# Performance work log

Measured on AMD Instinct MI355X. Metric: run time of the kernel, lower is better.

## Reference

```python
import jax, jax.numpy as jnp
import numpy as np

N_QUBITS = 16
N_LAYERS = 6
BATCH = 512


def _apply_1q(state, U, q, n, batched):
    """Apply a single-qubit gate U to qubit q of state (B, 2**n).
    U: (2,2) shared, or (B,2,2) per-sample if batched."""
    B = state.shape[0]
    d0, d1 = 2 ** q, 2 ** (n - q - 1)
    s = state.reshape(B, d0, 2, d1)
    if batched:
        s = jnp.einsum('bij,bxjy->bxiy', U, s)
    else:
        s = jnp.einsum('ij,bxjy->bxiy', U, s)
    return s.reshape(B, -1)


def _apply_cnot(state, c, t, n):
    """CNOT with control c, target t on state (B, 2**n)."""
    B = state.shape[0]
    a, b = (c, t) if c < t else (t, c)
    d0, d1, d2 = 2 ** a, 2 ** (b - a - 1), 2 ** (n - b - 1)
    s = state.reshape(B, d0, 2, d1, 2, d2)
    if c < t:  # control = axis 2, target = axis 4: flip target where control==1
        s = jnp.concatenate([s[:, :, :1], jnp.flip(s[:, :, 1:], axis=4)], axis=2)
    else:      # control = axis 4, target = axis 2
        s = jnp.concatenate([s[:, :, :, :, :1], jnp.flip(s[:, :, :, :, 1:], axis=2)], axis=4)
    return s.reshape(B, -1)


def _rx(theta):
    """RX(theta) for a batch of angles -> (B,2,2) complex64."""
    c = jnp.cos(theta * 0.5).astype(jnp.complex64)
    s = (-1j * jnp.sin(theta * 0.5)).astype(jnp.complex64)
    return jnp.stack([jnp.stack([c, s], -1), jnp.stack([s, c], -1)], -2)


def _rot(phi, theta, omega):
    """PennyLane Rot(phi,theta,omega) = RZ(omega) RY(theta) RZ(phi) -> (2,2) complex64."""
    c = jnp.cos(theta * 0.5)
    s = jnp.sin(theta * 0.5)
    m00 = jnp.exp(-0.5j * (phi + omega)) * c
    m01 = -jnp.exp(0.5j * (phi - omega)) * s
    m10 = jnp.exp(-0.5j * (phi - omega)) * s
    m11 = jnp.exp(0.5j * (phi + omega)) * c
    return jnp.stack([jnp.stack([m00, m01]), jnp.stack([m10, m11])]).astype(jnp.complex64)


def _circuit(x, weights, n, n_layers):
    B = x.shape[0]
    state = jnp.zeros((B, 2 ** n), dtype=jnp.complex64).at[:, 0].set(1.0)
    # AngleEmbedding: default rotation is RX(x_q) on wire q (per-sample angles)
    for q in range(n):
        state = _apply_1q(state, _rx(x[:, q]), q, n, batched=True)
    # StronglyEntanglingLayers: Rot on each wire, then ring of CNOTs with range r
    for l in range(n_layers):
        for q in range(n):
            U = _rot(weights[l, q, 0], weights[l, q, 1], weights[l, q, 2])
            state = _apply_1q(state, U, q, n, batched=False)
        r = (l % (n - 1)) + 1  # PennyLane default ranges
        for q in range(n):
            state = _apply_cnot(state, q, (q + r) % n, n)
    # <Z_q> = P(bit_q = 0) - P(bit_q = 1)
    probs = state.real ** 2 + state.imag ** 2  # (B, 2**n)
    exps = []
    for q in range(n):
        p = probs.reshape(B, 2 ** q, 2, -1).sum(axis=(1, 3))  # (B, 2)
        exps.append(p[:, 0] - p[:, 1])
    return jnp.stack(exps, axis=-1)  # (B, n)


def setup_inputs() -> dict:
    key = jax.random.key(0)
    kx, kw = jax.random.split(key)
    x = jax.random.normal(kx, (BATCH, N_QUBITS), dtype=jnp.float32)
    weights = jax.random.normal(kw, (N_LAYERS, N_QUBITS, 3), dtype=jnp.float32)
    return {"x": x, "weights": weights}


def reference(x, weights):
    return _circuit(x, weights, N_QUBITS, N_LAYERS)
```

## Files before the change

### kernel.cpp

```cpp
#include <hip/hip_runtime.h>


#define NTH 512
typedef float v32f __attribute__((ext_vector_type(32)));

template <int I> struct IC { static constexpr int value = I; };
template <int N, int I = 0, typename F>
__device__ __forceinline__ void static_for(F&& f) {
  if constexpr (I < N) { f(IC<I>{}); static_for<N, I + 1>(f); }
}


template <int LB>
__device__ __forceinline__ void rot_local(v32f& ar, v32f& ai, const float* __restrict__ u) {
  const float u00r = u[0], u00i = u[1], u01r = u[2], u01i = u[3];
  const float u10r = u[4], u10i = u[5], u11r = u[6], u11i = u[7];
  static_for<16>([&](auto hc) {
    constexpr int h = hc.value;
    constexpr int e0 = ((h >> LB) << (LB + 1)) | (h & ((1 << LB) - 1));
    constexpr int e1 = e0 | (1 << LB);
    const float axr = ar[e0], axi = ai[e0], bxr = ar[e1], bxi = ai[e1];
    ar[e0] = u00r * axr - u00i * axi + u01r * bxr - u01i * bxi;
    ai[e0] = u00r * axi + u00i * axr + u01r * bxi + u01i * bxr;
    ar[e1] = u10r * axr - u10i * axi + u11r * bxr - u11i * bxi;
    ai[e1] = u10r * axi + u10i * axr + u11r * bxi + u11i * bxr;
  });
}

__device__ __forceinline__ void rot_lane(v32f& ar, v32f& ai, const float* __restrict__ u,
                                         const int m, const int bit) {
  const float car = bit ? u[6] : u[0], cai = bit ? u[7] : u[1];
  const float cbr = bit ? u[4] : u[2], cbi = bit ? u[5] : u[3];
  static_for<32>([&](auto ec) {
    constexpr int e = ec.value;
    const float orr = ar[e], oii = ai[e];
    const float pr = __shfl_xor(orr, m);
    const float pi = __shfl_xor(oii, m);
    ar[e] = car * orr - cai * oii + cbr * pr - cbi * pi;
    ai[e] = car * oii + cai * orr + cbr * pi + cbi * pr;
  });
}

template <int TB, int LOCALLO, int C>
__device__ __forceinline__ void cnot_local(v32f& ar, v32f& ai, const int ibase) {
  static_for<16>([&](auto hc) {
    constexpr int h = hc.value;
    constexpr int e0 = ((h >> TB) << (TB + 1)) | (h & ((1 << TB) - 1));
    constexpr int e1 = e0 | (1 << TB);
    if constexpr (C >= LOCALLO && C < LOCALLO + 5) {
      if constexpr ((e0 >> (C - LOCALLO)) & 1) {
        const float tr = ar[e0], ti = ai[e0];
        ar[e0] = ar[e1]; ai[e0] = ai[e1];
        ar[e1] = tr;     ai[e1] = ti;
      }
    } else {
      const int take = (ibase >> C) & 1;
      const float axr = ar[e0], axi = ai[e0], bxr = ar[e1], bxi = ai[e1];
      ar[e0] = take ? bxr : axr; ai[e0] = take ? bxi : axi;
      ar[e1] = take ? axr : bxr; ai[e1] = take ? axi : bxi;
    }
  });
}

template <int LOCALLO, int C>
__device__ __forceinline__ void cnot_lane(v32f& ar, v32f& ai, const int m, const int ibase) {
  if constexpr (C >= LOCALLO && C < LOCALLO + 5) {
    static_for<32>([&](auto ec) {
      constexpr int e = ec.value;
      if constexpr ((e >> (C - LOCALLO)) & 1) {
        ar[e] = __shfl_xor(ar[e], m);
        ai[e] = __shfl_xor(ai[e], m);
      }
    });
  } else {
    const int take = (ibase >> C) & 1;
    static_for<32>([&](auto ec) {
      constexpr int e = ec.value;
      const float pr = __shfl_xor(ar[e], m);
      const float pi = __shfl_xor(ai[e], m);
      ar[e] = take ? pr : ar[e];
      ai[e] = take ? pi : ai[e];
    });
  }
}

__global__ void qsim_prep(const float* __restrict__ w, float* __restrict__ gm) {
  const int i = threadIdx.x;
  if (i < 96) {
    const float phi = w[i * 3 + 0];
    const float th  = w[i * 3 + 1];
    const float om  = w[i * 3 + 2];
    float st, ct; sincosf(0.5f * th, &st, &ct);
    float sa, ca; sincosf(0.5f * (phi + om), &sa, &ca);
    float sb, cb; sincosf(0.5f * (phi - om), &sb, &cb);
    float* u = gm + i * 8;
    u[0] =  ct * ca; u[1] = -ct * sa;
    u[2] = -st * cb; u[3] = -st * sb;
    u[4] =  st * cb; u[5] = -st * sb;
    u[6] =  ct * ca; u[7] =  ct * sa;
  }
}

template <int L>
__global__ void __launch_bounds__(NTH) sweepP(float2* __restrict__ st,
                                              const float* __restrict__ x,
                                              const float* __restrict__ gm) {
  const int tid = threadIdx.x;
  const int s  = blockIdx.x >> 2;
  const int fb = blockIdx.x & 3;
  const int ibase = (((tid >> 3) & 7) << 5) | (((tid >> 6) & 7) << 8) |
                    (fb << 11) | ((tid & 7) << 13);
  const int pbase = (((tid >> 3) & 7) << 1) | ((tid & 7) << 4) |
                    (((tid >> 6) & 7) << 11) | (fb << 14);
  float2* __restrict__ base = st + (s << 16) + pbase;
  constexpr int r = L + 1;
  const float* __restrict__ gl = gm + L * 128;
  v32f ar, ai;

  if constexpr (L == 0) {
    __shared__ float iv[16][4];
    if (tid < 16) {
      const float* u = gm + tid * 8;
      float sx, cx; sincosf(0.5f * x[s * 16 + tid], &sx, &cx);
      iv[tid][0] = u[0] * cx + u[3] * sx;
      iv[tid][1] = u[1] * cx - u[2] * sx;
      iv[tid][2] = u[4] * cx + u[7] * sx;
      iv[tid][3] = u[5] * cx - u[6] * sx;
    }
    __syncthreads();
    float Tr = 1.f, Ti = 0.f;
    #pragma unroll
    for (int b = 5; b <= 15; ++b) {
      const int bit = (ibase >> b) & 1;
      const float fr = iv[b][2 * bit], fi = iv[b][2 * bit + 1];
      const float nr = Tr * fr - Ti * fi; Ti = Tr * fi + Ti * fr; Tr = nr;
    }
    ar[0] = Tr; ai[0] = Ti;
    static_for<5>([&](auto bc) {
      constexpr int bI = bc.value;
      const float v0r = iv[bI][0], v0i = iv[bI][1], v1r = iv[bI][2], v1i = iv[bI][3];
      static_for<(1 << bI)>([&](auto kc) {
        constexpr int k = kc.value;
        constexpr int k1 = k | (1 << bI);
        const float kr = ar[k], ki = ai[k];
        ar[k1] = kr * v1r - ki * v1i; ai[k1] = kr * v1i + ki * v1r;
        ar[k]  = kr * v0r - ki * v0i; ai[k]  = kr * v0i + ki * v0r;
      });
    });
  } else {
    #pragma unroll
    for (int eh = 0; eh < 16; ++eh) {
      const float4 v = *reinterpret_cast<const float4*>(base + (eh << 7));
      ar[2 * eh] = v.x; ai[2 * eh] = v.y; ar[2 * eh + 1] = v.z; ai[2 * eh + 1] = v.w;
    }
    static_for<L>([&](auto kc) {
      constexpr int k = kc.value;
      constexpr int C = 16 - L + k;
      if constexpr (k <= 4) cnot_local<k, 0, C>(ar, ai, ibase);
      else                  cnot_lane<0, C>(ar, ai, 8, ibase);
    });
    rot_local<0>(ar, ai, gl);
    rot_local<1>(ar, ai, gl + 8);
    rot_local<2>(ar, ai, gl + 16);
    rot_local<3>(ar, ai, gl + 24);
    rot_local<4>(ar, ai, gl + 32);
    rot_lane(ar, ai, gl + 40, 8,  (tid >> 3) & 1);
    rot_lane(ar, ai, gl + 48, 16, (tid >> 4) & 1);
    rot_lane(ar, ai, gl + 56, 32, (tid >> 5) & 1);
  }

  static_for<8 - r>([&](auto gc) {
    constexpr int g = gc.value;
    constexpr int t = g + r;
    if constexpr (t <= 4) cnot_local<t, 0, g>(ar, ai, ibase);
    else                  cnot_lane<0, g>(ar, ai, 1 << (t - 2), ibase);
  });

  #pragma unroll
  for (int eh = 0; eh < 16; ++eh)
    *reinterpret_cast<float4*>(base + (eh << 7)) =
        make_float4(ar[2 * eh], ai[2 * eh], ar[2 * eh + 1], ai[2 * eh + 1]);
}

template <int L>
__global__ void __launch_bounds__(NTH) sweepQ(float2* __restrict__ st,
                                              const float* __restrict__ gm) {
  const int tid = threadIdx.x;
  const int s  = blockIdx.x >> 2;
  const int fb = blockIdx.x & 3;
  const int ibase = ((tid >> 6) & 7) | (fb << 3) | ((tid & 7) << 5) |
                    (((tid >> 3) & 7) << 13);
  const int pbase = ((tid >> 6) & 1) | ((tid & 7) << 1) | (((tid >> 3) & 7) << 4) |
                    (((tid >> 7) & 1) << 7) | (((tid >> 8) & 1) << 8) |
                    ((fb & 1) << 9) | (((fb >> 1) & 1) << 10);
  float2* __restrict__ base = st + (s << 16) + pbase;
  constexpr int r = L + 1;
  const float* __restrict__ gl = gm + L * 128;
  v32f ar, ai;
  #pragma unroll
  for (int e = 0; e < 32; ++e) {
    const float2 v = base[e << 11];
    ar[e] = v.x; ai[e] = v.y;
  }
  if constexpr (L > 0) {
    rot_local<0>(ar, ai, gl + 64);
    rot_local<1>(ar, ai, gl + 72);
    rot_local<2>(ar, ai, gl + 80);
    rot_local<3>(ar, ai, gl + 88);
    rot_local<4>(ar, ai, gl + 96);
    rot_lane(ar, ai, gl + 104, 8,  (tid >> 3) & 1);
    rot_lane(ar, ai, gl + 112, 16, (tid >> 4) & 1);
    rot_lane(ar, ai, gl + 120, 32, (tid >> 5) & 1);
  }
  static_for<8>([&](auto gc) {
    constexpr int g = 8 - r + gc.value;
    constexpr int t = g + r;
    if constexpr (t <= 12) cnot_local<t - 8, 8, g>(ar, ai, ibase);
    else                   cnot_lane<8, g>(ar, ai, 1 << (t - 10), ibase);
  });

  #pragma unroll
  for (int e = 0; e < 32; ++e) {
    float2 v; v.x = ar[e]; v.y = ai[e];
    base[e << 11] = v;
  }
}

__global__ void __launch_bounds__(NTH) finalK(const float2* __restrict__ st,
                                              float* __restrict__ part) {
  const int tid = threadIdx.x;
  const int s  = blockIdx.x >> 2;
  const int fb = blockIdx.x & 3;
  const int ibase = (((tid >> 3) & 7) << 5) | (((tid >> 6) & 7) << 8) |
                    (fb << 11) | ((tid & 7) << 13);
  const int pbase = (((tid >> 3) & 7) << 1) | ((tid & 7) << 4) |
                    (((tid >> 6) & 7) << 11) | (fb << 14);
  const float2* __restrict__ base = st + (s << 16) + pbase;
  v32f ar, ai;
  #pragma unroll
  for (int eh = 0; eh < 16; ++eh) {
    const float4 v = *reinterpret_cast<const float4*>(base + (eh << 7));
    ar[2 * eh] = v.x; ai[2 * eh] = v.y; ar[2 * eh + 1] = v.z; ai[2 * eh + 1] = v.w;
  }
  static_for<6>([&](auto kc) {
    constexpr int k = kc.value;
    constexpr int C = 10 + k;
    if constexpr (k <= 4) cnot_local<k, 0, C>(ar, ai, ibase);
    else                  cnot_lane<0, C>(ar, ai, 8, ibase);
  });
  __shared__ float red[8][16];
  float tot = 0.f, sl0 = 0.f, sl1 = 0.f, sl2 = 0.f, sl3 = 0.f, sl4 = 0.f;
  static_for<32>([&](auto ec) {
    constexpr int e = ec.value;
    const float p = ar[e] * ar[e] + ai[e] * ai[e];
    tot += p;
    if constexpr (e & 1)  sl0 -= p; else sl0 += p;
    if constexpr (e & 2)  sl1 -= p; else sl1 += p;
    if constexpr (e & 4)  sl2 -= p; else sl2 += p;
    if constexpr (e & 8)  sl3 -= p; else sl3 += p;
    if constexpr (e & 16) sl4 -= p; else sl4 += p;
  });
  const float sl[5] = {sl0, sl1, sl2, sl3, sl4};
  const int wv = tid >> 6;
  static_for<16>([&](auto qc) {
    constexpr int q = qc.value;
    float v;
    if constexpr (q < 5) v = sl[q];
    else v = ((ibase >> q) & 1) ? -tot : tot;
    v += __shfl_xor(v, 1);  v += __shfl_xor(v, 2);  v += __shfl_xor(v, 4);
    v += __shfl_xor(v, 8);  v += __shfl_xor(v, 16); v += __shfl_xor(v, 32);
    if ((tid & 63) == 0) red[wv][q] = v;
  });
  __syncthreads();
  if (tid < 16) {
    float a = 0.f;
    #pragma unroll
    for (int w8 = 0; w8 < 8; ++w8) a += red[w8][tid];
    part[blockIdx.x * 16 + tid] = a;
  }
}

__global__ void __launch_bounds__(NTH) reduceK(const float* __restrict__ part,
                                               float* __restrict__ out) {
  const int j = blockIdx.x * NTH + threadIdx.x;
  const int s = j >> 4, q = j & 15;
  float a = 0.f;
  #pragma unroll
  for (int f = 0; f < 4; ++f) a += part[(s << 6) + f * 16 + q];
  out[j] = a;
}

extern "C" void kernel_launch(void* const* d_in, const int* in_sizes, int n_in,
                              void* d_out, int out_size, void* d_ws, size_t ws_size,
                              hipStream_t stream) {
  (void)in_sizes; (void)n_in; (void)out_size;
  const float* x = (const float*)d_in[0];
  const float* w = (const float*)d_in[1];
  float* out = (float*)d_out;
  float* gm   = (float*)d_ws;
  float* part = (float*)((char*)d_ws + 4096);
  float2* st  = (float2*)((char*)d_ws + 524288);

  const size_t avail = ws_size > 524288 ? ws_size - 524288 : 0;
  long long chunk = (long long)(avail / 524288);
  if (chunk > 256) chunk = 256;
  if (chunk < 1) chunk = 1;

  qsim_prep<<<dim3(1), dim3(128), 0, stream>>>(w, gm);
  for (int s0 = 0; s0 < 512; s0 += (int)chunk) {
    const int ns = (512 - s0) < (int)chunk ? (512 - s0) : (int)chunk;
    const dim3 g(ns * 4), b(NTH);
    const float* xs = x + s0 * 16;
    float* pp = part + (size_t)s0 * 64;
    sweepP<0><<<g, b, 0, stream>>>(st, xs, gm);
    sweepQ<0><<<g, b, 0, stream>>>(st, gm);
    sweepP<1><<<g, b, 0, stream>>>(st, xs, gm);
    sweepQ<1><<<g, b, 0, stream>>>(st, gm);
    sweepP<2><<<g, b, 0, stream>>>(st, xs, gm);
    sweepQ<2><<<g, b, 0, stream>>>(st, gm);
    sweepP<3><<<g, b, 0, stream>>>(st, xs, gm);
    sweepQ<3><<<g, b, 0, stream>>>(st, gm);
    sweepP<4><<<g, b, 0, stream>>>(st, xs, gm);
    sweepQ<4><<<g, b, 0, stream>>>(st, gm);
    sweepP<5><<<g, b, 0, stream>>>(st, xs, gm);
    sweepQ<5><<<g, b, 0, stream>>>(st, gm);
    finalK<<<g, b, 0, stream>>>(st, pp);
  }
  reduceK<<<dim3(16), dim3(NTH), 0, stream>>>(part, out);
}
```

Measured before the change: 1.770 ms.

## Widen sweepQ to two adjacent amplitudes per thread with float4 accesses

sweepQ now gives each thread 64 amplitudes: two adjacent states along the lowest qubit, each with 32 elements. Loads and stores become 16-byte float4 instead of strided 8-byte float2, and the grid shrinks to two blocks per sample. The intent is better memory coalescing and transaction efficiency in the high-qubit sweep, plus fewer blocks. In exchange, register pressure roughly doubles (128 floats of state per thread at 512 threads), which risks spills or lower occupancy.

```diff
diff --git a/kernel.cpp b/kernel.cpp
--- a/kernel.cpp
+++ b/kernel.cpp
@@ -41,14 +41,14 @@
   });
 }
 
-template <int TB, int LOCALLO, int C>
-__device__ __forceinline__ void cnot_local(v32f& ar, v32f& ai, const int ibase) {
+template <int TB, int C>
+__device__ __forceinline__ void cnot_localP(v32f& ar, v32f& ai, const int ibase) {
   static_for<16>([&](auto hc) {
     constexpr int h = hc.value;
     constexpr int e0 = ((h >> TB) << (TB + 1)) | (h & ((1 << TB) - 1));
     constexpr int e1 = e0 | (1 << TB);
-    if constexpr (C >= LOCALLO && C < LOCALLO + 5) {
-      if constexpr ((e0 >> (C - LOCALLO)) & 1) {
+    if constexpr (C < 5) {
+      if constexpr ((e0 >> C) & 1) {
         const float tr = ar[e0], ti = ai[e0];
         ar[e0] = ar[e1]; ai[e0] = ai[e1];
         ar[e1] = tr;     ai[e1] = ti;
@@ -62,12 +62,12 @@
   });
 }
 
-template <int LOCALLO, int C>
-__device__ __forceinline__ void cnot_lane(v32f& ar, v32f& ai, const int m, const int ibase) {
-  if constexpr (C >= LOCALLO && C < LOCALLO + 5) {
+template <int C>
+__device__ __forceinline__ void cnot_laneP(v32f& ar, v32f& ai, const int m, const int ibase) {
+  if constexpr (C < 5) {
     static_for<32>([&](auto ec) {
       constexpr int e = ec.value;
-      if constexpr ((e >> (C - LOCALLO)) & 1) {
+      if constexpr ((e >> C) & 1) {
         ar[e] = __shfl_xor(ar[e], m);
         ai[e] = __shfl_xor(ai[e], m);
       }
@@ -80,6 +80,108 @@
       const float pi = __shfl_xor(ai[e], m);
       ar[e] = take ? pr : ar[e];
       ai[e] = take ? pi : ai[e];
+    });
+  }
+}
+
+
+template <int J>
+__device__ __forceinline__ void rot_m(v32f& ar0, v32f& ai0, v32f& ar1, v32f& ai1,
+                                      const float* __restrict__ u) {
+  const float u00r = u[0], u00i = u[1], u01r = u[2], u01i = u[3];
+  const float u10r = u[4], u10i = u[5], u11r = u[6], u11i = u[7];
+  static_for<16>([&](auto hc) {
+    constexpr int h = hc.value;
+    constexpr int m0 = ((h >> J) << (J + 1)) | (h & ((1 << J) - 1));
+    constexpr int m1 = m0 | (1 << J);
+    {
+      const float axr = ar0[m0], axi = ai0[m0], bxr = ar0[m1], bxi = ai0[m1];
+      ar0[m0] = u00r * axr - u00i * axi + u01r * bxr - u01i * bxi;
+      ai0[m0] = u00r * axi + u00i * axr + u01r * bxi + u01i * bxr;
+      ar0[m1] = u10r * axr - u10i * axi + u11r * bxr - u11i * bxi;
+      ai0[m1] = u10r * axi + u10i * axr + u11r * bxi + u11i * bxr;
+    }
+    {
+      const float axr = ar1[m0], axi = ai1[m0], bxr = ar1[m1], bxi = ai1[m1];
+      ar1[m0] = u00r * axr - u00i * axi + u01r * bxr - u01i * bxi;
+      ai1[m0] = u00r * axi + u00i * axr + u01r * bxi + u01i * bxr;
+      ar1[m1] = u10r * axr - u10i * axi + u11r * bxr - u11i * bxi;
+      ai1[m1] = u10r * axi + u10i * axr + u11r * bxi + u11i * bxr;
+    }
+  });
+}
+
+__device__ __forceinline__ void rot_laneQ(v32f& ar0, v32f& ai0, v32f& ar1, v32f& ai1,
+                                          const float* __restrict__ u,
+                                          const int m, const int bit) {
+  const float car = bit ? u[6] : u[0], cai = bit ? u[7] : u[1];
+  const float cbr = bit ? u[4] : u[2], cbi = bit ? u[5] : u[3];
+  static_for<32>([&](auto ec) {
+    constexpr int e = ec.value;
+    {
+      const float orr = ar0[e], oii = ai0[e];
+      const float pr = __shfl_xor(orr, m);
+      const float pi = __shfl_xor(oii, m);
+      ar0[e] = car * orr - cai * oii + cbr * pr - cbi * pi;
+      ai0[e] = car * oii + cai * orr + cbr * pi + cbi * pr;
+    }
+    {
+      const float orr = ar1[e], oii = ai1[e];
+      const float pr = __shfl_xor(orr, m);
+      const float pi = __shfl_xor(oii, m);
+      ar1[e] = car * orr - cai * oii + cbr * pr - cbi * pi;
+      ai1[e] = car * oii + cai * orr + cbr * pi + cbi * pr;
+    }
+  });
+}
+
+template <int J, int C>
+__device__ __forceinline__ void cnot_mQ(v32f& ar0, v32f& ai0, v32f& ar1, v32f& ai1,
+                                        const int ibase) {
+  constexpr int SB = (C >= 8 && C <= 12) ? (C - 8) : -1;
+  static_for<16>([&](auto hc) {
+    constexpr int h = hc.value;
+    constexpr int m0 = ((h >> J) << (J + 1)) | (h & ((1 << J) - 1));
+    constexpr int m1 = m0 | (1 << J);
+    if constexpr (SB >= 0) {
+      if constexpr ((m0 >> SB) & 1) {
+        { const float tr = ar0[m0], ti = ai0[m0];
+          ar0[m0] = ar0[m1]; ai0[m0] = ai0[m1]; ar0[m1] = tr; ai0[m1] = ti; }
+        { const float tr = ar1[m0], ti = ai1[m0];
+          ar1[m0] = ar1[m1]; ai1[m0] = ai1[m1]; ar1[m1] = tr; ai1[m1] = ti; }
+      }
+    } else {
+      const int take = (ibase >> C) & 1;
+      { const float axr = ar0[m0], axi = ai0[m0], bxr = ar0[m1], bxi = ai0[m1];
+        ar0[m0] = take ? bxr : axr; ai0[m0] = take ? bxi : axi;
+        ar0[m1] = take ? axr : bxr; ai0[m1] = take ? axi : bxi; }
+      { const float axr = ar1[m0], axi = ai1[m0], bxr = ar1[m1], bxi = ai1[m1];
+        ar1[m0] = take ? bxr : axr; ai1[m0] = take ? bxi : axi;
+        ar1[m1] = take ? axr : bxr; ai1[m1] = take ? axi : bxi; }
+    }
+  });
+}
+
+template <int C>
+__device__ __forceinline__ void cnot_laneQ(v32f& ar0, v32f& ai0, v32f& ar1, v32f& ai1,
+                                           const int m, const int ibase) {
+  constexpr int SB = (C >= 8 && C <= 12) ? (C - 8) : -1;
+  if constexpr (SB >= 0) {
+    static_for<32>([&](auto ec) {
+      constexpr int e = ec.value;
+      if constexpr ((e >> SB) & 1) {
+        ar0[e] = __shfl_xor(ar0[e], m); ai0[e] = __shfl_xor(ai0[e], m);
+        ar1[e] = __shfl_xor(ar1[e], m); ai1[e] = __shfl_xor(ai1[e], m);
+      }
+    });
+  } else {
+    const int take = (ibase >> C) & 1;
+    static_for<32>([&](auto ec) {
+      constexpr int e = ec.value;
+      { const float pr = __shfl_xor(ar0[e], m), pi = __shfl_xor(ai0[e], m);
+        ar0[e] = take ? pr : ar0[e]; ai0[e] = take ? pi : ai0[e]; }
+      { const float pr = __shfl_xor(ar1[e], m), pi = __shfl_xor(ai1[e], m);
+        ar1[e] = take ? pr : ar1[e]; ai1[e] = take ? pi : ai1[e]; }
     });
   }
 }
@@ -156,8 +258,7 @@
     static_for<L>([&](auto kc) {
       constexpr int k = kc.value;
       constexpr int C = 16 - L + k;
-      if constexpr (k <= 4) cnot_local<k, 0, C>(ar, ai, ibase);
-      else                  cnot_lane<0, C>(ar, ai, 8, ibase);
+      cnot_localP<k, C>(ar, ai, ibase);
     });
     rot_local<0>(ar, ai, gl);
     rot_local<1>(ar, ai, gl + 8);
@@ -172,8 +273,8 @@
   static_for<8 - r>([&](auto gc) {
     constexpr int g = gc.value;
     constexpr int t = g + r;
-    if constexpr (t <= 4) cnot_local<t, 0, g>(ar, ai, ibase);
-    else                  cnot_lane<0, g>(ar, ai, 1 << (t - 2), ibase);
+    if constexpr (t <= 4) cnot_localP<t, g>(ar, ai, ibase);
+    else                  cnot_laneP<g>(ar, ai, 1 << (t - 2), ibase);
   });
 
   #pragma unroll
@@ -186,44 +287,42 @@
 __global__ void __launch_bounds__(NTH) sweepQ(float2* __restrict__ st,
                                               const float* __restrict__ gm) {
   const int tid = threadIdx.x;
-  const int s  = blockIdx.x >> 2;
-  const int fb = blockIdx.x & 3;
-  const int ibase = ((tid >> 6) & 7) | (fb << 3) | ((tid & 7) << 5) |
-                    (((tid >> 3) & 7) << 13);
-  const int pbase = ((tid >> 6) & 1) | ((tid & 7) << 1) | (((tid >> 3) & 7) << 4) |
-                    (((tid >> 7) & 1) << 7) | (((tid >> 8) & 1) << 8) |
-                    ((fb & 1) << 9) | (((fb >> 1) & 1) << 10);
+  const int s  = blockIdx.x >> 1;
+  const int fb = blockIdx.x & 1;
+  const int ibase = ((tid & 7) << 5) | (((tid >> 3) & 7) << 13) |
+                    (((tid >> 6) & 7) << 1) | (fb << 4);
+  const int pbase = ((tid & 7) << 1) | (((tid >> 3) & 7) << 4) |
+                    (((tid >> 6) & 7) << 7) | (fb << 10);
   float2* __restrict__ base = st + (s << 16) + pbase;
   constexpr int r = L + 1;
   const float* __restrict__ gl = gm + L * 128;
-  v32f ar, ai;
+  v32f ar0, ai0, ar1, ai1;
   #pragma unroll
-  for (int e = 0; e < 32; ++e) {
-    const float2 v = base[e << 11];
-    ar[e] = v.x; ai[e] = v.y;
+  for (int m = 0; m < 32; ++m) {
+    const float4 v = *reinterpret_cast<const float4*>(base + (m << 11));
+    ar0[m] = v.x; ai0[m] = v.y; ar1[m] = v.z; ai1[m] = v.w;
   }
   if constexpr (L > 0) {
-    rot_local<0>(ar, ai, gl + 64);
-    rot_local<1>(ar, ai, gl + 72);
-    rot_local<2>(ar, ai, gl + 80);
-    rot_local<3>(ar, ai, gl + 88);
-    rot_local<4>(ar, ai, gl + 96);
-    rot_lane(ar, ai, gl + 104, 8,  (tid >> 3) & 1);
-    rot_lane(ar, ai, gl + 112, 16, (tid >> 4) & 1);
-    rot_lane(ar, ai, gl + 120, 32, (tid >> 5) & 1);
+    rot_m<0>(ar0, ai0, ar1, ai1, gl + 64);
+    rot_m<1>(ar0, ai0, ar1, ai1, gl + 72);
+    rot_m<2>(ar0, ai0, ar1, ai1, gl + 80);
+    rot_m<3>(ar0, ai0, ar1, ai1, gl + 88);
+    rot_m<4>(ar0, ai0, ar1, ai1, gl + 96);
+    rot_laneQ(ar0, ai0, ar1, ai1, gl + 104, 8,  (tid >> 3) & 1);
+    rot_laneQ(ar0, ai0, ar1, ai1, gl + 112, 16, (tid >> 4) & 1);
+    rot_laneQ(ar0, ai0, ar1, ai1, gl + 120, 32, (tid >> 5) & 1);
   }
   static_for<8>([&](auto gc) {
     constexpr int g = 8 - r + gc.value;
     constexpr int t = g + r;
-    if constexpr (t <= 12) cnot_local<t - 8, 8, g>(ar, ai, ibase);
-    else                   cnot_lane<8, g>(ar, ai, 1 << (t - 10), ibase);
+    if constexpr (t <= 12) cnot_mQ<t - 8, g>(ar0, ai0, ar1, ai1, ibase);
+    else                   cnot_laneQ<g>(ar0, ai0, ar1, ai1, 1 << (t - 10), ibase);
   });
 
   #pragma unroll
-  for (int e = 0; e < 32; ++e) {
-    float2 v; v.x = ar[e]; v.y = ai[e];
-    base[e << 11] = v;
-  }
+  for (int m = 0; m < 32; ++m)
+    *reinterpret_cast<float4*>(base + (m << 11)) =
+        make_float4(ar0[m], ai0[m], ar1[m], ai1[m]);
 }
 
 __global__ void __launch_bounds__(NTH) finalK(const float2* __restrict__ st,
@@ -245,8 +344,8 @@
   static_for<6>([&](auto kc) {
     constexpr int k = kc.value;
     constexpr int C = 10 + k;
-    if constexpr (k <= 4) cnot_local<k, 0, C>(ar, ai, ibase);
-    else                  cnot_lane<0, C>(ar, ai, 8, ibase);
+    if constexpr (k <= 4) cnot_localP<k, C>(ar, ai, ibase);
+    else                  cnot_laneP<C>(ar, ai, 8, ibase);
   });
   __shared__ float red[8][16];
   float tot = 0.f, sl0 = 0.f, sl1 = 0.f, sl2 = 0.f, sl3 = 0.f, sl4 = 0.f;
@@ -309,22 +408,22 @@
   qsim_prep<<<dim3(1), dim3(128), 0, stream>>>(w, gm);
   for (int s0 = 0; s0 < 512; s0 += (int)chunk) {
     const int ns = (512 - s0) < (int)chunk ? (512 - s0) : (int)chunk;
-    const dim3 g(ns * 4), b(NTH);
+    const dim3 gp(ns * 4), gq(ns * 2), b(NTH);
     const float* xs = x + s0 * 16;
     float* pp = part + (size_t)s0 * 64;
-    sweepP<0><<<g, b, 0, stream>>>(st, xs, gm);
-    sweepQ<0><<<g, b, 0, stream>>>(st, gm);
-    sweepP<1><<<g, b, 0, stream>>>(st, xs, gm);
-    sweepQ<1><<<g, b, 0, stream>>>(st, gm);
-    sweepP<2><<<g, b, 0, stream>>>(st, xs, gm);
-    sweepQ<2><<<g, b, 0, stream>>>(st, gm);
-    sweepP<3><<<g, b, 0, stream>>>(st, xs, gm);
-    sweepQ<3><<<g, b, 0, stream>>>(st, gm);
-    sweepP<4><<<g, b, 0, stream>>>(st, xs, gm);
-    sweepQ<4><<<g, b, 0, stream>>>(st, gm);
-    sweepP<5><<<g, b, 0, stream>>>(st, xs, gm);
-    sweepQ<5><<<g, b, 0, stream>>>(st, gm);
-    finalK<<<g, b, 0, stream>>>(st, pp);
+    sweepP<0><<<gp, b, 0, stream>>>(st, xs, gm);
+    sweepQ<0><<<gq, b, 0, stream>>>(st, gm);
+    sweepP<1><<<gp, b, 0, stream>>>(st, xs, gm);
+    sweepQ<1><<<gq, b, 0, stream>>>(st, gm);
+    sweepP<2><<<gp, b, 0, stream>>>(st, xs, gm);
+    sweepQ<2><<<gq, b, 0, stream>>>(st, gm);
+    sweepP<3><<<gp, b, 0, stream>>>(st, xs, gm);
+    sweepQ<3><<<gq, b, 0, stream>>>(st, gm);
+    sweepP<4><<<gp, b, 0, stream>>>(st, xs, gm);
+    sweepQ<4><<<gq, b, 0, stream>>>(st, gm);
+    sweepP<5><<<gp, b, 0, stream>>>(st, xs, gm);
+    sweepQ<5><<<gq, b, 0, stream>>>(st, gm);
+    finalK<<<gp, b, 0, stream>>>(st, pp);
   }
   reduceK<<<dim3(16), dim3(NTH), 0, stream>>>(part, out);
 }
```

Measured after the change: 5.009 ms. 2.83x slower.

## Change state storage permutation so cross-sweep CNOTs stay register-local

Applied to the files above, without the earlier changes.

Changes the physical index permutation of the state vector shared by the P, Q and final sweep kernels. P-sweep elements now sit at stride 64 and load as float2 instead of float4 pairs. This lets the carried-over CNOTs use register-local swaps instead of cross-lane shuffles. The cost is narrower, less vectorized global loads and stores in the P and final kernels, while the Q kernel gets a simpler contiguous lane mapping.

```diff
diff --git a/kernel.cpp b/kernel.cpp
--- a/kernel.cpp
+++ b/kernel.cpp
@@ -110,7 +110,7 @@
   const int fb = blockIdx.x & 3;
   const int ibase = (((tid >> 3) & 7) << 5) | (((tid >> 6) & 7) << 8) |
                     (fb << 11) | ((tid & 7) << 13);
-  const int pbase = (((tid >> 3) & 7) << 1) | ((tid & 7) << 4) |
+  const int pbase = ((tid >> 3) & 7) | ((tid & 7) << 3) |
                     (((tid >> 6) & 7) << 11) | (fb << 14);
   float2* __restrict__ base = st + (s << 16) + pbase;
   constexpr int r = L + 1;
@@ -149,15 +149,14 @@
     });
   } else {
     #pragma unroll
-    for (int eh = 0; eh < 16; ++eh) {
-      const float4 v = *reinterpret_cast<const float4*>(base + (eh << 7));
-      ar[2 * eh] = v.x; ai[2 * eh] = v.y; ar[2 * eh + 1] = v.z; ai[2 * eh + 1] = v.w;
+    for (int e = 0; e < 32; ++e) {
+      const float2 v = base[e << 6];
+      ar[e] = v.x; ai[e] = v.y;
     }
     static_for<L>([&](auto kc) {
       constexpr int k = kc.value;
       constexpr int C = 16 - L + k;
-      if constexpr (k <= 4) cnot_local<k, 0, C>(ar, ai, ibase);
-      else                  cnot_lane<0, C>(ar, ai, 8, ibase);
+      cnot_local<k, 0, C>(ar, ai, ibase);
     });
     rot_local<0>(ar, ai, gl);
     rot_local<1>(ar, ai, gl + 8);
@@ -177,9 +176,10 @@
   });
 
   #pragma unroll
-  for (int eh = 0; eh < 16; ++eh)
-    *reinterpret_cast<float4*>(base + (eh << 7)) =
-        make_float4(ar[2 * eh], ai[2 * eh], ar[2 * eh + 1], ai[2 * eh + 1]);
+  for (int e = 0; e < 32; ++e) {
+    float2 v; v.x = ar[e]; v.y = ai[e];
+    base[e << 6] = v;
+  }
 }
 
 template <int L>
@@ -190,9 +190,8 @@
   const int fb = blockIdx.x & 3;
   const int ibase = ((tid >> 6) & 7) | (fb << 3) | ((tid & 7) << 5) |
                     (((tid >> 3) & 7) << 13);
-  const int pbase = ((tid >> 6) & 1) | ((tid & 7) << 1) | (((tid >> 3) & 7) << 4) |
-                    (((tid >> 7) & 1) << 7) | (((tid >> 8) & 1) << 8) |
-                    ((fb & 1) << 9) | (((fb >> 1) & 1) << 10);
+  const int pbase = (tid & 7) | (((tid >> 3) & 7) << 3) |
+                    (((tid >> 6) & 7) << 6) | (fb << 9);
   float2* __restrict__ base = st + (s << 16) + pbase;
   constexpr int r = L + 1;
   const float* __restrict__ gl = gm + L * 128;
@@ -233,14 +232,14 @@
   const int fb = blockIdx.x & 3;
   const int ibase = (((tid >> 3) & 7) << 5) | (((tid >> 6) & 7) << 8) |
                     (fb << 11) | ((tid & 7) << 13);
-  const int pbase = (((tid >> 3) & 7) << 1) | ((tid & 7) << 4) |
+  const int pbase = ((tid >> 3) & 7) | ((tid & 7) << 3) |
                     (((tid >> 6) & 7) << 11) | (fb << 14);
   const float2* __restrict__ base = st + (s << 16) + pbase;
   v32f ar, ai;
   #pragma unroll
-  for (int eh = 0; eh < 16; ++eh) {
-    const float4 v = *reinterpret_cast<const float4*>(base + (eh << 7));
-    ar[2 * eh] = v.x; ai[2 * eh] = v.y; ar[2 * eh + 1] = v.z; ai[2 * eh + 1] = v.w;
+  for (int e = 0; e < 32; ++e) {
+    const float2 v = base[e << 6];
+    ar[e] = v.x; ai[e] = v.y;
   }
   static_for<6>([&](auto kc) {
     constexpr int k = kc.value;
```

Measured after the change: 1.714 ms. 1.03x faster.
